# Kernel optimization log

Hardware: AMD Instinct MI355X
Metric: run time of the kernel (lower is better)

The kernel has to match this reference:

```python
import jax, jax.numpy as jnp
import numpy as np

LAT_T, LAT_H, LAT_W = 16, 44, 80  # hard-coded latent grid in preprocess_mask


def _preprocess_mask(mask):
    """mask: [T, H, W, B] float video mask -> [B, S] binary mask, S = 16*44*80.
    Mirrors torch trilinear interpolate (align_corners=False) per temporal chunk."""
    m = jnp.transpose(mask, (3, 0, 1, 2))[:, None]  # [B,1,T,H,W]
    B, _, T, _, _ = m.shape
    tgt = (B, 1, 1, LAT_H, LAT_W)
    pieces = [jax.image.resize(m[:, :, :1], tgt, 'trilinear', antialias=False)]
    for wi in range(1, T, 8):
        pieces.append(jax.image.resize(m[:, :, wi:wi + 8], tgt, 'trilinear', antialias=False))
    mm = jnp.concatenate(pieces, axis=2)[:, 0]  # [B,16,44,80]
    return (mm > 0.5).astype(jnp.float32).reshape(B, -1)  # [B,S]


def setup_inputs() -> dict:
    key = jax.random.key(0)
    ks = jax.random.split(key, 6)
    B, S, H, D, P, R = 1, 56320, 8, 64, 128, 2
    T, MH, MW = 121, 88, 160
    return {
        'q': jax.random.normal(ks[0], (B, S, H, D), jnp.float32),
        'k': jax.random.normal(ks[1], (B, P, H, D), jnp.float32),
        'v': jax.random.normal(ks[2], (B, P, H, D), jnp.float32),
        'regional_k': jax.random.normal(ks[3], (R, B, P, H, D), jnp.float32),
        'regional_v': jax.random.normal(ks[4], (R, B, P, H, D), jnp.float32),
        'region_masks': jax.random.uniform(ks[5], (R, T, MH, MW, B), jnp.float32),
    }


def reference(q, k, v, regional_k, regional_v, region_masks):
    B, S, H, D = q.shape
    P = k.shape[1]
    R = regional_k.shape[0]
    scale = D ** -0.5
    base_ratio = 0.5

    # per-region binary masks over the latent sequence: [R,B,S]
    masks = jnp.stack([_preprocess_mask(region_masks[i]) for i in range(R)], axis=0)
    masks_b = masks > 0.5
    global_mask = masks.sum(axis=0) == 0  # [B,S] queries covered by no region
    # allowed[b,s,r]: segment r of combined KV (r=0 global prompt, r>=1 region r-1)
    allowed = jnp.concatenate([global_mask[..., None], jnp.moveaxis(masks_b, 0, -1)], axis=-1)  # [B,S,R+1]

    combined_k = jnp.concatenate([k[None], regional_k], axis=0)  # [R+1,B,P,H,D]
    combined_v = jnp.concatenate([v[None], regional_v], axis=0)

    # regional pass: scores [B,H,S,R+1,P], additive -inf bias per segment
    scores = jnp.einsum('bshd,rbphd->bhsrp', q, combined_k) * scale
    scores = jnp.where(allowed[:, None, :, :, None], scores, -jnp.inf)
    p = jax.nn.softmax(scores.reshape(B, H, S, (R + 1) * P), axis=-1)
    out_reg = jnp.einsum('bhsrp,rbphd->bshd', p.reshape(B, H, S, R + 1, P), combined_v)

    # base pass: plain cross attention over the global prompt
    s_base = jnp.einsum('bshd,bphd->bhsp', q, k) * scale
    out_base = jnp.einsum('bhsp,bphd->bshd', jax.nn.softmax(s_base, axis=-1), v)

    out = out_reg * (1.0 - base_ratio) + out_base * base_ratio
    return out.reshape(B, S, H * D)
```

## Files before the change

### kernel.cpp

```cpp
#include <hip/hip_runtime.h>

typedef short short8  __attribute__((ext_vector_type(8)));
typedef short short4v __attribute__((ext_vector_type(4)));
typedef float f32x4   __attribute__((ext_vector_type(4)));

#define MFMA_BF16(A,B,C) __builtin_amdgcn_mfma_f32_16x16x32_bf16((A),(B),(C),0,0,0)

__device__ __forceinline__ short bf16bits(float f){
  return (short)__builtin_bit_cast(unsigned short, static_cast<__bf16>(f));
}

#define EXP_SCORE(s) __builtin_amdgcn_exp2f(__builtin_fmaf((s), 0.18033688011112042f, -11.541560327111707f))

__global__ __launch_bounds__(256) void prep_kernel(const float* __restrict__ rm,
                                                   const float* __restrict__ k,
                                                   const float* __restrict__ v,
                                                   const float* __restrict__ rk,
                                                   const float* __restrict__ rv,
                                                   unsigned* __restrict__ allowed,
                                                   unsigned short* __restrict__ Kb,
                                                   unsigned short* __restrict__ VT){
  const int bid = blockIdx.x;
  if (bid < 220){
    int s = bid*256 + threadIdx.x;
    if (s >= 56320) return;
    int t = s / 3520;
    int rem = s - t*3520;
    int i = rem / 80;
    int j = rem - i*80;
    int y = 2*i, x = 2*j;
    bool bin[2];
    #pragma unroll
    for (int r=0;r<2;r++){
      const float* base = rm + (size_t)r*121*88*160;
      float acc;
      if (t == 0){
        const float* p0 = base + (size_t)(0*88 + y)*160 + x;
        acc = 0.25f*(p0[0]+p0[1]+p0[160]+p0[161]);
      } else {
        const float* pa = base + (size_t)((8*t-4)*88 + y)*160 + x;
        const float* pb = base + (size_t)((8*t-3)*88 + y)*160 + x;
        acc = 0.125f*(pa[0]+pa[1]+pa[160]+pa[161] + pb[0]+pb[1]+pb[160]+pb[161]);
      }
      bin[r] = acc > 0.5f;
    }
    unsigned bits = (bin[0]||bin[1]) ? 0u : 1u;
    if (bin[0]) bits |= 2u;
    if (bin[1]) bits |= 4u;
    allowed[s] = bits;
  } else {
    int idx = (bid-220)*256 + threadIdx.x;
    if (idx >= 3*128*8*64) return;
    int d   = idx & 63;
    int h   = (idx >> 6) & 7;
    int p   = (idx >> 9) & 127;
    int seg = idx >> 16;
    int low = idx & 65535;
    float kv_, vv_;
    if (seg == 0){ kv_ = k[low];                          vv_ = v[low]; }
    else         { kv_ = rk[(size_t)(seg-1)*65536 + low]; vv_ = rv[(size_t)(seg-1)*65536 + low]; }
    const int kk = seg*128 + p;
    Kb[(size_t)h*24576 + ((kk>>4)*2 + (d>>5))*512
       + ((((d>>3)&3)*16) + (kk&15))*8 + (d&7)] = (unsigned short)bf16bits(kv_);
    VT[(size_t)h*24576 + ((kk>>5)*4 + (d>>4))*512
       + ((((kk>>3)&3)*16) + (d&15))*8 + (kk&7)] = (unsigned short)bf16bits(vv_);
  }
}

__global__ __launch_bounds__(512)
void attn_kernel(const float* __restrict__ q,
                 const unsigned* __restrict__ allowed,
                 const unsigned short* __restrict__ Kb,
                 const unsigned short* __restrict__ VT,
                 float* __restrict__ out){
  const int h    = blockIdx.y;
  const int wave = threadIdx.x >> 6;
  const int lane = threadIdx.x & 63;
  const int c    = lane & 15;
  const int Q    = lane >> 4;

  __shared__ __align__(16) char Ks[49152];
  __shared__ __align__(16) char Ps[16384];

  const int s = blockIdx.x*128 + wave*16 + c;

  const char* kg = (const char*)Kb + (size_t)h*49152;
  short8 st0 = *(const short8*)(kg + wave*6144 + 0*1024 + lane*16);
  short8 st1 = *(const short8*)(kg + wave*6144 + 1*1024 + lane*16);
  short8 st2 = *(const short8*)(kg + wave*6144 + 2*1024 + lane*16);
  short8 st3 = *(const short8*)(kg + wave*6144 + 3*1024 + lane*16);
  short8 st4 = *(const short8*)(kg + wave*6144 + 4*1024 + lane*16);
  short8 st5 = *(const short8*)(kg + wave*6144 + 5*1024 + lane*16);

  const unsigned ab = allowed[s];
  const float* qp = q + ((size_t)s*8 + h)*64 + Q*8;
  f32x4 q0 = *(const f32x4*)(qp);
  f32x4 q1 = *(const f32x4*)(qp+4);
  f32x4 q2 = *(const f32x4*)(qp+32);
  f32x4 q3 = *(const f32x4*)(qp+36);
  short8 f0, f1;
  #pragma unroll
  for (int j=0;j<4;j++){
    f0[j] = bf16bits(q0[j]); f0[4+j] = bf16bits(q1[j]);
    f1[j] = bf16bits(q2[j]); f1[4+j] = bf16bits(q3[j]);
  }

  *(short8*)(Ks + wave*6144 + 0*1024 + lane*16) = st0;
  *(short8*)(Ks + wave*6144 + 1*1024 + lane*16) = st1;
  *(short8*)(Ks + wave*6144 + 2*1024 + lane*16) = st2;
  *(short8*)(Ks + wave*6144 + 3*1024 + lane*16) = st3;
  *(short8*)(Ks + wave*6144 + 4*1024 + lane*16) = st4;
  *(short8*)(Ks + wave*6144 + 5*1024 + lane*16) = st5;

  const char* kfb = Ks + lane*16;
  const char* vgf = (const char*)VT + (size_t)h*49152 + lane*16;
  char*       pwb = Ps + wave*2048 + (Q>>1)*256 + c*16 + (Q&1)*8;
  const char* prb = Ps + wave*2048 + lane*16;

  short8 v0, v1, v2, v3, v4, v5, v6, v7;
#define VLOAD(ph)                                                     \
  v0 = *(const short8*)(vgf + (((ph)*2+0)*4+0)*1024);                 \
  v1 = *(const short8*)(vgf + (((ph)*2+0)*4+1)*1024);                 \
  v2 = *(const short8*)(vgf + (((ph)*2+0)*4+2)*1024);                 \
  v3 = *(const short8*)(vgf + (((ph)*2+0)*4+3)*1024);                 \
  v4 = *(const short8*)(vgf + (((ph)*2+1)*4+0)*1024);                 \
  v5 = *(const short8*)(vgf + (((ph)*2+1)*4+1)*1024);                 \
  v6 = *(const short8*)(vgf + (((ph)*2+1)*4+2)*1024);                 \
  v7 = *(const short8*)(vgf + (((ph)*2+1)*4+3)*1024);                 \
  __builtin_amdgcn_sched_barrier(0);

#define DO_SCORES(ph, LSUM, AM)                                       \
  {                                                                   \
    _Pragma("unroll")                                                 \
    for (int i=0;i<4;i++){                                            \
      const int t = (ph)*4 + i;                                       \
      short8 kf0 = *(const short8*)(kfb + (t*2  )*1024);              \
      short8 kf1 = *(const short8*)(kfb + (t*2+1)*1024);              \
      f32x4 s4 = {0,0,0,0};                                           \
      s4 = MFMA_BF16(kf0,f0,s4); s4 = MFMA_BF16(kf1,f1,s4);           \
      short4v pk;                                                     \
      _Pragma("unroll")                                               \
      for (int r=0;r<4;r++){                                          \
        float e = (AM)*EXP_SCORE(s4[r]); LSUM += e;                   \
        pk[r] = bf16bits(e);                                          \
      }                                                               \
      *(short4v*)(pwb + i*512) = pk;                                  \
    }                                                                 \
  }

#define DO_PV(ACC)                                                    \
  {                                                                   \
    short8 pf0 = *(const short8*)(prb);                               \
    short8 pf1 = *(const short8*)(prb + 1024);                        \
    ACC[0] = MFMA_BF16(v0, pf0, ACC[0]);                              \
    ACC[1] = MFMA_BF16(v1, pf0, ACC[1]);                              \
    ACC[2] = MFMA_BF16(v2, pf0, ACC[2]);                              \
    ACC[3] = MFMA_BF16(v3, pf0, ACC[3]);                              \
    ACC[0] = MFMA_BF16(v4, pf1, ACC[0]);                              \
    ACC[1] = MFMA_BF16(v5, pf1, ACC[1]);                              \
    ACC[2] = MFMA_BF16(v6, pf1, ACC[2]);                              \
    ACC[3] = MFMA_BF16(v7, pf1, ACC[3]);                              \
  }

  VLOAD(0);

  __syncthreads();

  const float am1 = (ab>>1)&1u ? 1.f : 0.f;
  const float am2 = (ab>>2)&1u ? 1.f : 0.f;

  float lb=0.f, lr=0.f;
  f32x4 a0[4], a1[4];
  #pragma unroll
  for (int m=0;m<4;m++){ a0[m]=(f32x4){0,0,0,0}; a1[m]=(f32x4){0,0,0,0}; }

  DO_SCORES(0, lb, 1.0f);  DO_PV(a0);  VLOAD(1);
  DO_SCORES(1, lb, 1.0f);  DO_PV(a0);  VLOAD(2);
  DO_SCORES(2, lr, am1);   DO_PV(a1);  VLOAD(3);
  DO_SCORES(3, lr, am1);   DO_PV(a1);  VLOAD(4);
  DO_SCORES(4, lr, am2);   DO_PV(a1);  VLOAD(5);
  DO_SCORES(5, lr, am2);   DO_PV(a1);

  lb += __shfl_xor(lb,16); lb += __shfl_xor(lb,32);
  lr += __shfl_xor(lr,16); lr += __shfl_xor(lr,32);

  const float invb = 0.5f/lb;
  const float lreg = ((ab&1u)? lb : 0.f) + lr;
  const float invr = 0.5f/lreg;
  const float cA   = invb + ((ab&1u)? invr : 0.f);

  float* ob = out + (size_t)s*512 + h*64 + Q*4;
  #pragma unroll
  for (int m=0;m<4;m++){
    f32x4 o;
    #pragma unroll
    for (int r=0;r<4;r++) o[r] = a0[m][r]*cA + a1[m][r]*invr;
    *(f32x4*)(ob + m*16) = o;
  }
}

extern "C" void kernel_launch(void* const* d_in, const int* in_sizes, int n_in,
                              void* d_out, int out_size, void* d_ws, size_t ws_size,
                              hipStream_t stream) {
  const float* q  = (const float*)d_in[0];
  const float* k  = (const float*)d_in[1];
  const float* v  = (const float*)d_in[2];
  const float* rk = (const float*)d_in[3];
  const float* rv = (const float*)d_in[4];
  const float* rm = (const float*)d_in[5];
  float* out = (float*)d_out;

  char* ws = (char*)d_ws;
  unsigned*       allowed = (unsigned*)ws;
  unsigned short* Kb      = (unsigned short*)(ws + 225280);
  unsigned short* VT      = (unsigned short*)(ws + 225280 + 393216);

  prep_kernel<<<988, 256, 0, stream>>>(rm, k, v, rk, rv, allowed, Kb, VT);
  dim3 grid(440, 8);
  attn_kernel<<<grid, 512, 0, stream>>>(q, allowed, Kb, VT, out);
}
```

Baseline: 266.3 us.

## Keep softmax probabilities in registers by permuting V layout to match MFMA output

Permutes the bf16 V-transpose layout written by the prep kernel so that score MFMA outputs can feed the PV MFMA B-operand directly from registers. This removes the per-wave LDS staging buffer for P, along with its writes and reads. The loop is restructured into 12 chunks of 32 keys, each running two score MFMA pairs, the exponentials, and four PV MFMAs. In exchange it shrinks V prefetch granularity and makes the dependency chain per chunk tighter.

```diff
diff --git a/kernel.cpp b/kernel.cpp
--- a/kernel.cpp
+++ b/kernel.cpp
@@ -62,8 +62,13 @@
     const int kk = seg*128 + p;
     Kb[(size_t)h*24576 + ((kk>>4)*2 + (d>>5))*512
        + ((((d>>3)&3)*16) + (kk&15))*8 + (d&7)] = (unsigned short)bf16bits(kv_);
-    VT[(size_t)h*24576 + ((kk>>5)*4 + (d>>4))*512
-       + ((((kk>>3)&3)*16) + (d&15))*8 + (kk&7)] = (unsigned short)bf16bits(vv_);
+    {
+      const int kkc = kk & 31;
+      const int Qv  = (kkc >> 2) & 3;
+      const int jv  = (kkc & 3) | ((kkc & 16) >> 2);
+      VT[(size_t)h*24576 + ((kk>>5)*4 + (d>>4))*512
+         + (Qv*16 + (d&15))*8 + jv] = (unsigned short)bf16bits(vv_);
+    }
   }
 }
 
@@ -80,7 +85,6 @@
   const int Q    = lane >> 4;
 
   __shared__ __align__(16) char Ks[49152];
-  __shared__ __align__(16) char Ps[16384];
 
   const int s = blockIdx.x*128 + wave*16 + c;
 
@@ -114,52 +118,33 @@
 
   const char* kfb = Ks + lane*16;
   const char* vgf = (const char*)VT + (size_t)h*49152 + lane*16;
-  char*       pwb = Ps + wave*2048 + (Q>>1)*256 + c*16 + (Q&1)*8;
-  const char* prb = Ps + wave*2048 + lane*16;
-
-  short8 v0, v1, v2, v3, v4, v5, v6, v7;
-#define VLOAD(ph)                                                     \
-  v0 = *(const short8*)(vgf + (((ph)*2+0)*4+0)*1024);                 \
-  v1 = *(const short8*)(vgf + (((ph)*2+0)*4+1)*1024);                 \
-  v2 = *(const short8*)(vgf + (((ph)*2+0)*4+2)*1024);                 \
-  v3 = *(const short8*)(vgf + (((ph)*2+0)*4+3)*1024);                 \
-  v4 = *(const short8*)(vgf + (((ph)*2+1)*4+0)*1024);                 \
-  v5 = *(const short8*)(vgf + (((ph)*2+1)*4+1)*1024);                 \
-  v6 = *(const short8*)(vgf + (((ph)*2+1)*4+2)*1024);                 \
-  v7 = *(const short8*)(vgf + (((ph)*2+1)*4+3)*1024);                 \
+
+  short8 v0, v1, v2, v3;
+#define VLOAD(kc)                                                     \
+  v0 = *(const short8*)(vgf + ((kc)*4+0)*1024);                       \
+  v1 = *(const short8*)(vgf + ((kc)*4+1)*1024);                       \
+  v2 = *(const short8*)(vgf + ((kc)*4+2)*1024);                       \
+  v3 = *(const short8*)(vgf + ((kc)*4+3)*1024);                       \
   __builtin_amdgcn_sched_barrier(0);
 
-#define DO_SCORES(ph, LSUM, AM)                                       \
+#define CHUNK(kc, LSUM, AM, ACC)                                      \
   {                                                                   \
+    short8 kf0 = *(const short8*)(kfb + ((kc)*4+0)*1024);             \
+    short8 kf1 = *(const short8*)(kfb + ((kc)*4+1)*1024);             \
+    short8 kf2 = *(const short8*)(kfb + ((kc)*4+2)*1024);             \
+    short8 kf3 = *(const short8*)(kfb + ((kc)*4+3)*1024);             \
+    f32x4 sA = {0,0,0,0}; sA = MFMA_BF16(kf0,f0,sA); sA = MFMA_BF16(kf1,f1,sA); \
+    f32x4 sB = {0,0,0,0}; sB = MFMA_BF16(kf2,f0,sB); sB = MFMA_BF16(kf3,f1,sB); \
+    short8 pf;                                                        \
     _Pragma("unroll")                                                 \
-    for (int i=0;i<4;i++){                                            \
-      const int t = (ph)*4 + i;                                       \
-      short8 kf0 = *(const short8*)(kfb + (t*2  )*1024);              \
-      short8 kf1 = *(const short8*)(kfb + (t*2+1)*1024);              \
-      f32x4 s4 = {0,0,0,0};                                           \
-      s4 = MFMA_BF16(kf0,f0,s4); s4 = MFMA_BF16(kf1,f1,s4);           \
-      short4v pk;                                                     \
-      _Pragma("unroll")                                               \
-      for (int r=0;r<4;r++){                                          \
-        float e = (AM)*EXP_SCORE(s4[r]); LSUM += e;                   \
-        pk[r] = bf16bits(e);                                          \
-      }                                                               \
-      *(short4v*)(pwb + i*512) = pk;                                  \
+    for (int r=0;r<4;r++){                                            \
+      float eA = (AM)*EXP_SCORE(sA[r]); LSUM += eA; pf[r]   = bf16bits(eA); \
+      float eB = (AM)*EXP_SCORE(sB[r]); LSUM += eB; pf[4+r] = bf16bits(eB); \
     }                                                                 \
-  }
-
-#define DO_PV(ACC)                                                    \
-  {                                                                   \
-    short8 pf0 = *(const short8*)(prb);                               \
-    short8 pf1 = *(const short8*)(prb + 1024);                        \
-    ACC[0] = MFMA_BF16(v0, pf0, ACC[0]);                              \
-    ACC[1] = MFMA_BF16(v1, pf0, ACC[1]);                              \
-    ACC[2] = MFMA_BF16(v2, pf0, ACC[2]);                              \
-    ACC[3] = MFMA_BF16(v3, pf0, ACC[3]);                              \
-    ACC[0] = MFMA_BF16(v4, pf1, ACC[0]);                              \
-    ACC[1] = MFMA_BF16(v5, pf1, ACC[1]);                              \
-    ACC[2] = MFMA_BF16(v6, pf1, ACC[2]);                              \
-    ACC[3] = MFMA_BF16(v7, pf1, ACC[3]);                              \
+    ACC[0] = MFMA_BF16(v0, pf, ACC[0]);                               \
+    ACC[1] = MFMA_BF16(v1, pf, ACC[1]);                               \
+    ACC[2] = MFMA_BF16(v2, pf, ACC[2]);                               \
+    ACC[3] = MFMA_BF16(v3, pf, ACC[3]);                               \
   }
 
   VLOAD(0);
@@ -174,12 +159,18 @@
   #pragma unroll
   for (int m=0;m<4;m++){ a0[m]=(f32x4){0,0,0,0}; a1[m]=(f32x4){0,0,0,0}; }
 
-  DO_SCORES(0, lb, 1.0f);  DO_PV(a0);  VLOAD(1);
-  DO_SCORES(1, lb, 1.0f);  DO_PV(a0);  VLOAD(2);
-  DO_SCORES(2, lr, am1);   DO_PV(a1);  VLOAD(3);
-  DO_SCORES(3, lr, am1);   DO_PV(a1);  VLOAD(4);
-  DO_SCORES(4, lr, am2);   DO_PV(a1);  VLOAD(5);
-  DO_SCORES(5, lr, am2);   DO_PV(a1);
+  CHUNK(0,  lb, 1.0f, a0); VLOAD(1);
+  CHUNK(1,  lb, 1.0f, a0); VLOAD(2);
+  CHUNK(2,  lb, 1.0f, a0); VLOAD(3);
+  CHUNK(3,  lb, 1.0f, a0); VLOAD(4);
+  CHUNK(4,  lr, am1,  a1); VLOAD(5);
+  CHUNK(5,  lr, am1,  a1); VLOAD(6);
+  CHUNK(6,  lr, am1,  a1); VLOAD(7);
+  CHUNK(7,  lr, am1,  a1); VLOAD(8);
+  CHUNK(8,  lr, am2,  a1); VLOAD(9);
+  CHUNK(9,  lr, am2,  a1); VLOAD(10);
+  CHUNK(10, lr, am2,  a1); VLOAD(11);
+  CHUNK(11, lr, am2,  a1);
 
   lb += __shfl_xor(lb,16); lb += __shfl_xor(lb,32);
   lr += __shfl_xor(lr,16); lr += __shfl_xor(lr,32);
```

After: 264.7 us. About the same (-0.6%).
